# Kernel optimization log

Hardware: AMD Instinct MI355X
Metric: run time of the kernel (lower is better)

## Reference

```python
import jax, jax.numpy as jnp
import numpy as np
import math

ALPHA = math.exp(-0.001 * 1000.0)  # exp(-dt * tau_filter_inv)
T, B, D_IN, D_OUT = 2048, 32, 512, 512


def setup_inputs() -> dict:
    key = jax.random.key(0)
    k1, k2, k3 = jax.random.split(key, 3)
    bound = 1.0 / math.sqrt(D_IN)  # torch Linear default init range
    return {
        "input_tensor": jax.random.normal(k1, (T, B, D_IN), dtype=jnp.float32),
        "weight": jax.random.uniform(k2, (D_OUT, D_IN), minval=-bound, maxval=bound, dtype=jnp.float32),
        "bias": jax.random.uniform(k3, (D_OUT,), minval=-bound, maxval=bound, dtype=jnp.float32),
    }


def reference(input_tensor, weight, bias):
    # y[t] = W x[t] + b   -> [T, B, D_OUT]
    y = jnp.einsum("tbi,oi->tbo", input_tensor, weight) + bias
    alpha = jnp.asarray(ALPHA, dtype=y.dtype)

    # out[0] = y[0]; out[t] = alpha * out[t-1] + y[t]
    def step(carry, yt):
        out = alpha * carry + yt
        return out, out

    _, rest = jax.lax.scan(step, y[0], y[1:])
    return jnp.concatenate([y[:1], rest], axis=0)
```

## Files before the change

kernel.cpp:

```cpp
#include <hip/hip_runtime.h>
#include <stdint.h>

#define T_DIM 2048
#define B_DIM 32
#define DIN   512
#define DOUT  512
#define M_DIM (T_DIM * B_DIM)
#define COLS  (B_DIM * DIN)
#define COLS4 (COLS / 4)

#define ALPHA_F 0.36787944117144233f
#define INV_1MA 1.5819767068693265f

#define CHUNKS   128
#define CHUNK_T  16
#define HALO     8

#define FCHUNKS  32
#define FCHUNK_T 64
#define FHALO    16

typedef float  floatx4 __attribute__((ext_vector_type(4)));
typedef __bf16 bf16x8  __attribute__((ext_vector_type(8)));

__device__ __forceinline__ uint32_t pk2(float a, float b) {
  uint32_t ua = __float_as_uint(a); ua += 0x7fffu + ((ua >> 16) & 1u);
  uint32_t ub = __float_as_uint(b); ub += 0x7fffu + ((ub >> 16) & 1u);
  return (ua >> 16) | (ub & 0xffff0000u);
}

__device__ __forceinline__ void gload_lds16(const void* g, void* lds) {
  __builtin_amdgcn_global_load_lds(
      (const __attribute__((address_space(1))) void*)g,
      (__attribute__((address_space(3))) void*)lds,
      16, 0, 0);
}

__global__ void filter_x_kernel(const float* __restrict__ X,
                                uint16_t* __restrict__ XF,
                                const float* __restrict__ W,
                                uint16_t* __restrict__ WB)
{
  if (blockIdx.y == CHUNKS) {
    const int t = blockIdx.x * 256 + threadIdx.x;
    const float4* W4 = (const float4*)W;
#pragma unroll
    for (int j = 0; j < 8; ++j) {
      const int b4 = t * 16 + j * 2;
      float4 w0 = W4[b4], w1 = W4[b4 + 1];
      uint4 p;
      p.x = pk2(w0.x, w0.y); p.y = pk2(w0.z, w0.w);
      p.z = pk2(w1.x, w1.y); p.w = pk2(w1.z, w1.w);
      *(uint4*)&WB[t * 64 + j * 8] = p;
    }
    return;
  }

  const int col4 = blockIdx.x * blockDim.x + threadIdx.x;
  const int c = blockIdx.y;
  const float4* X4 = (const float4*)X;

  const size_t base = (size_t)c * CHUNK_T * COLS4 + col4;

  float4 h[HALO];
  float4 v[CHUNK_T];

  if (c > 0) {
    const size_t hb = base - (size_t)HALO * COLS4;
#pragma unroll
    for (int j = 0; j < HALO; ++j) h[j] = X4[hb + (size_t)j * COLS4];
  }
#pragma unroll
  for (int j = 0; j < CHUNK_T; ++j) v[j] = X4[base + (size_t)j * COLS4];

  float4 carry = {0.0f, 0.0f, 0.0f, 0.0f};
  if (c > 0) {
#pragma unroll
    for (int j = 0; j < HALO; ++j) {
      carry.x = fmaf(ALPHA_F, carry.x, h[j].x);
      carry.y = fmaf(ALPHA_F, carry.y, h[j].y);
      carry.z = fmaf(ALPHA_F, carry.z, h[j].z);
      carry.w = fmaf(ALPHA_F, carry.w, h[j].w);
    }
  }

#pragma unroll
  for (int j = 0; j < CHUNK_T; ++j) {
    carry.x = fmaf(ALPHA_F, carry.x, v[j].x);
    carry.y = fmaf(ALPHA_F, carry.y, v[j].y);
    carry.z = fmaf(ALPHA_F, carry.z, v[j].z);
    carry.w = fmaf(ALPHA_F, carry.w, v[j].w);
    uint2 p;
    p.x = pk2(carry.x, carry.y);
    p.y = pk2(carry.z, carry.w);
    *(uint2*)&XF[(base + (size_t)j * COLS4) * 4] = p;
  }
}

__launch_bounds__(256, 4)
__global__ void gemm_bf16_kernel(const uint16_t* __restrict__ XF,
                                 const uint16_t* __restrict__ WB,
                                 const float* __restrict__ bias,
                                 float* __restrict__ Y)
{
  __shared__ __align__(16) uint16_t As[128 * 64];
  __shared__ __align__(16) uint16_t Bs[128 * 64];

  const int bid = blockIdx.x;
  const int lg = (bid & 7) * 256 + (bid >> 3);
  const int n0 = (lg & 3) * 128;
  const int m0 = (lg >> 2) * 128;

  const int tid  = threadIdx.x;
  const int lane = tid & 63;
  const int w    = tid >> 6;
  const int r    = lane & 15;
  const int q    = lane >> 4;
  const int wm   = w >> 1;
  const int wn   = w & 1;

  const int srow_base = w * 32 + (lane >> 3);
  const int schunk    = lane & 7;

  floatx4 acc[4][4];
#pragma unroll
  for (int i = 0; i < 4; ++i)
#pragma unroll
    for (int j = 0; j < 4; ++j) {
      floatx4 z = {0.0f, 0.0f, 0.0f, 0.0f};
      acc[i][j] = z;
    }

  for (int kt = 0; kt < DIN / 64; ++kt) {
    const int k0 = kt * 64;
#pragma unroll
    for (int i = 0; i < 4; ++i) {
      const int row = srow_base + i * 8;
      const int sc = schunk ^ (row & 7);
      gload_lds16(XF + (size_t)(m0 + row) * DIN + k0 + sc * 8,
                  &As[(w * 32 + i * 8) * 64]);
      gload_lds16(WB + (size_t)(n0 + row) * DIN + k0 + sc * 8,
                  &Bs[(w * 32 + i * 8) * 64]);
    }
    __syncthreads();

#pragma unroll
    for (int kk = 0; kk < 2; ++kk) {
      bf16x8 af[4], bfr[4];
#pragma unroll
      for (int mi = 0; mi < 4; ++mi) {
        const int row = wm * 64 + mi * 16 + r;
        const int cch = (kk * 4 + q) ^ (row & 7);
        af[mi] = *(const bf16x8*)&As[row * 64 + (cch << 3)];
      }
#pragma unroll
      for (int ni = 0; ni < 4; ++ni) {
        const int row = wn * 64 + ni * 16 + r;
        const int cch = (kk * 4 + q) ^ (row & 7);
        bfr[ni] = *(const bf16x8*)&Bs[row * 64 + (cch << 3)];
      }
#pragma unroll
      for (int mi = 0; mi < 4; ++mi)
#pragma unroll
        for (int ni = 0; ni < 4; ++ni)
          acc[mi][ni] = __builtin_amdgcn_mfma_f32_16x16x32_bf16(
              af[mi], bfr[ni], acc[mi][ni], 0, 0, 0);
    }
    __syncthreads();
  }

#pragma unroll
  for (int mi = 0; mi < 4; ++mi) {
    const int rowb = m0 + wm * 64 + mi * 16;
    const int t = rowb >> 5;
    const float s = (1.0f - __expf(-(float)(t + 1))) * INV_1MA;
#pragma unroll
    for (int ni = 0; ni < 4; ++ni) {
      const int col = n0 + wn * 64 + ni * 16 + r;
      const float sb = s * bias[col];
#pragma unroll
      for (int j = 0; j < 4; ++j)
        Y[(size_t)(rowb + q * 4 + j) * DOUT + col] = acc[mi][ni][j] + sb;
    }
  }
}

__launch_bounds__(256, 2)
__global__ void gemm_bias_kernel(const float* __restrict__ X,
                                 const float* __restrict__ W,
                                 const float* __restrict__ bias,
                                 float* __restrict__ Y,
                                 float* __restrict__ halo,
                                 int halo_on)
{
  __shared__ __align__(16) uint16_t As[128 * 64];
  __shared__ __align__(16) uint16_t Bs[128 * 64];

  const int tid  = threadIdx.x;
  const int lane = tid & 63;
  const int wave = tid >> 6;
  const int wm   = wave >> 1;
  const int wn   = wave & 1;
  const int r    = lane & 15;
  const int q    = lane >> 4;

  const int m0 = blockIdx.y * 128;
  const int n0 = blockIdx.x * 128;

  floatx4 acc[4][4];
#pragma unroll
  for (int i = 0; i < 4; ++i)
#pragma unroll
    for (int j = 0; j < 4; ++j) {
      floatx4 z = {0.0f, 0.0f, 0.0f, 0.0f};
      acc[i][j] = z;
    }

  for (int kt = 0; kt < DIN / 64; ++kt) {
    const int k0 = kt * 64;
#pragma unroll
    for (int j = 0; j < 4; ++j) {
      const int cid = tid + j * 256;
      const int row = cid >> 3;
      const int c   = cid & 7;
      const int slot = (c ^ (row & 7)) << 3;

      const float* ga = &X[(size_t)(m0 + row) * DIN + k0 + c * 8];
      float4 a0 = *(const float4*)ga;
      float4 a1 = *(const float4*)(ga + 4);
      uint4 pa;
      pa.x = pk2(a0.x, a0.y); pa.y = pk2(a0.z, a0.w);
      pa.z = pk2(a1.x, a1.y); pa.w = pk2(a1.z, a1.w);
      *(uint4*)&As[row * 64 + slot] = pa;

      const float* gb = &W[(size_t)(n0 + row) * DIN + k0 + c * 8];
      float4 b0 = *(const float4*)gb;
      float4 b1 = *(const float4*)(gb + 4);
      uint4 pb;
      pb.x = pk2(b0.x, b0.y); pb.y = pk2(b0.z, b0.w);
      pb.z = pk2(b1.x, b1.y); pb.w = pk2(b1.z, b1.w);
      *(uint4*)&Bs[row * 64 + slot] = pb;
    }
    __syncthreads();

#pragma unroll
    for (int kk = 0; kk < 2; ++kk) {
      bf16x8 af[4], bfr[4];
#pragma unroll
      for (int mi = 0; mi < 4; ++mi) {
        const int row = wm * 64 + mi * 16 + r;
        const int c   = (kk * 4 + q) ^ (row & 7);
        af[mi] = *(const bf16x8*)&As[row * 64 + (c << 3)];
      }
#pragma unroll
      for (int ni = 0; ni < 4; ++ni) {
        const int row = wn * 64 + ni * 16 + r;
        const int c   = (kk * 4 + q) ^ (row & 7);
        bfr[ni] = *(const bf16x8*)&Bs[row * 64 + (c << 3)];
      }
#pragma unroll
      for (int mi = 0; mi < 4; ++mi)
#pragma unroll
        for (int ni = 0; ni < 4; ++ni)
          acc[mi][ni] = __builtin_amdgcn_mfma_f32_16x16x32_bf16(
              af[mi], bfr[ni], acc[mi][ni], 0, 0, 0);
    }
    __syncthreads();
  }

#pragma unroll
  for (int ni = 0; ni < 4; ++ni) {
    const int col = n0 + wn * 64 + ni * 16 + r;
    const float bv = bias[col];
#pragma unroll
    for (int mi = 0; mi < 4; ++mi) {
      const int rowm = m0 + wm * 64 + mi * 16 + q * 4;
      const int t = rowm >> 5;
      const int b = rowm & 31;
      const int tloc = t & (FCHUNK_T - 1);
      const bool hw = halo_on && (tloc >= FCHUNK_T - FHALO) && (t < T_DIM - FCHUNK_T);
      const size_t hbase = hw
          ? ((size_t)(((t >> 6) + 1) * FHALO + (tloc - (FCHUNK_T - FHALO))) * COLS)
          : 0;
#pragma unroll
      for (int j = 0; j < 4; ++j) {
        const float v = acc[mi][ni][j] + bv;
        Y[(size_t)(rowm + j) * DOUT + col] = v;
        if (hw) halo[hbase + (size_t)(b + j) * DOUT + col] = v;
      }
    }
  }
}

__global__ void scan_kernel(float* __restrict__ Y,
                            const float* __restrict__ halo,
                            int chunk_len)
{
  const int col4 = blockIdx.x * blockDim.x + threadIdx.x;
  const int c = blockIdx.y;

  float4* Y4 = (float4*)Y;
  const float4* H4 = (const float4*)halo;

  float4 carry = {0.0f, 0.0f, 0.0f, 0.0f};
  if (c > 0) {
#pragma unroll
    for (int h = 0; h < FHALO; ++h) {
      float4 v = H4[(size_t)(c * FHALO + h) * COLS4 + col4];
      carry.x = fmaf(ALPHA_F, carry.x, v.x);
      carry.y = fmaf(ALPHA_F, carry.y, v.y);
      carry.z = fmaf(ALPHA_F, carry.z, v.z);
      carry.w = fmaf(ALPHA_F, carry.w, v.w);
    }
  }

  size_t idx = (size_t)c * chunk_len * COLS4 + col4;
  float4 ynext = Y4[idx];
  for (int t = 0; t < chunk_len; ++t) {
    float4 y = ynext;
    if (t + 1 < chunk_len) ynext = Y4[idx + COLS4];
    carry.x = fmaf(ALPHA_F, carry.x, y.x);
    carry.y = fmaf(ALPHA_F, carry.y, y.y);
    carry.z = fmaf(ALPHA_F, carry.z, y.z);
    carry.w = fmaf(ALPHA_F, carry.w, y.w);
    Y4[idx] = carry;
    idx += COLS4;
  }
}

extern "C" void kernel_launch(void* const* d_in, const int* in_sizes, int n_in,
                              void* d_out, int out_size, void* d_ws, size_t ws_size,
                              hipStream_t stream)
{
  const float* X    = (const float*)d_in[0];
  const float* W    = (const float*)d_in[1];
  const float* bias = (const float*)d_in[2];
  float* Y = (float*)d_out;

  const size_t need_new = (size_t)M_DIM * DIN * 2 + (size_t)DOUT * DIN * 2;

  if (ws_size >= need_new) {
    uint16_t* XF = (uint16_t*)d_ws;
    uint16_t* WB = XF + (size_t)M_DIM * DIN;

    dim3 gf(16, CHUNKS + 1);
    filter_x_kernel<<<gf, 256, 0, stream>>>(X, XF, W, WB);

    gemm_bf16_kernel<<<2048, 256, 0, stream>>>(XF, WB, bias, Y);
  } else {
    float* halo = (float*)d_ws;
    const size_t halo_need = (size_t)FCHUNKS * FHALO * COLS * sizeof(float);
    const int halo_on = (ws_size >= halo_need) ? 1 : 0;

    dim3 g1(DOUT / 128, M_DIM / 128);
    gemm_bias_kernel<<<g1, 256, 0, stream>>>(X, W, bias, Y, halo, halo_on);

    const int n_chunks = halo_on ? FCHUNKS : 1;
    dim3 g2(COLS4 / 256, n_chunks);
    scan_kernel<<<g2, 256, 0, stream>>>(Y, halo, T_DIM / n_chunks);
  }
}
```

Baseline: 98.09 us.

## Fuse input prefilter into GEMM A-tile load, dropping the XF intermediate

```diff
diff --git a/kernel.cpp b/kernel.cpp
--- a/kernel.cpp
+++ b/kernel.cpp
@@ -12,9 +12,7 @@
 #define ALPHA_F 0.36787944117144233f
 #define INV_1MA 1.5819767068693265f
 
-#define CHUNKS   128
-#define CHUNK_T  16
-#define HALO     8
+#define HALO 8
 
 #define FCHUNKS  32
 #define FCHUNK_T 64
@@ -36,72 +34,27 @@
       16, 0, 0);
 }
 
-__global__ void filter_x_kernel(const float* __restrict__ X,
-                                uint16_t* __restrict__ XF,
-                                const float* __restrict__ W,
-                                uint16_t* __restrict__ WB)
-{
-  if (blockIdx.y == CHUNKS) {
-    const int t = blockIdx.x * 256 + threadIdx.x;
-    const float4* W4 = (const float4*)W;
-#pragma unroll
-    for (int j = 0; j < 8; ++j) {
-      const int b4 = t * 16 + j * 2;
-      float4 w0 = W4[b4], w1 = W4[b4 + 1];
-      uint4 p;
-      p.x = pk2(w0.x, w0.y); p.y = pk2(w0.z, w0.w);
-      p.z = pk2(w1.x, w1.y); p.w = pk2(w1.z, w1.w);
-      *(uint4*)&WB[t * 64 + j * 8] = p;
-    }
-    return;
-  }
-
-  const int col4 = blockIdx.x * blockDim.x + threadIdx.x;
-  const int c = blockIdx.y;
-  const float4* X4 = (const float4*)X;
-
-  const size_t base = (size_t)c * CHUNK_T * COLS4 + col4;
-
-  float4 h[HALO];
-  float4 v[CHUNK_T];
-
-  if (c > 0) {
-    const size_t hb = base - (size_t)HALO * COLS4;
-#pragma unroll
-    for (int j = 0; j < HALO; ++j) h[j] = X4[hb + (size_t)j * COLS4];
-  }
-#pragma unroll
-  for (int j = 0; j < CHUNK_T; ++j) v[j] = X4[base + (size_t)j * COLS4];
-
-  float4 carry = {0.0f, 0.0f, 0.0f, 0.0f};
-  if (c > 0) {
-#pragma unroll
-    for (int j = 0; j < HALO; ++j) {
-      carry.x = fmaf(ALPHA_F, carry.x, h[j].x);
-      carry.y = fmaf(ALPHA_F, carry.y, h[j].y);
-      carry.z = fmaf(ALPHA_F, carry.z, h[j].z);
-      carry.w = fmaf(ALPHA_F, carry.w, h[j].w);
-    }
-  }
-
-#pragma unroll
-  for (int j = 0; j < CHUNK_T; ++j) {
-    carry.x = fmaf(ALPHA_F, carry.x, v[j].x);
-    carry.y = fmaf(ALPHA_F, carry.y, v[j].y);
-    carry.z = fmaf(ALPHA_F, carry.z, v[j].z);
-    carry.w = fmaf(ALPHA_F, carry.w, v[j].w);
-    uint2 p;
-    p.x = pk2(carry.x, carry.y);
-    p.y = pk2(carry.z, carry.w);
-    *(uint2*)&XF[(base + (size_t)j * COLS4) * 4] = p;
-  }
-}
-
-__launch_bounds__(256, 4)
-__global__ void gemm_bf16_kernel(const uint16_t* __restrict__ XF,
-                                 const uint16_t* __restrict__ WB,
-                                 const float* __restrict__ bias,
-                                 float* __restrict__ Y)
+__global__ void wconv_kernel(const float* __restrict__ W,
+                             uint16_t* __restrict__ WB)
+{
+  const int t = blockIdx.x * 256 + threadIdx.x;
+  const float4* W4 = (const float4*)W;
+#pragma unroll
+  for (int j = 0; j < 8; ++j) {
+    const int b4 = t * 16 + j * 2;
+    float4 w0 = W4[b4], w1 = W4[b4 + 1];
+    uint4 p;
+    p.x = pk2(w0.x, w0.y); p.y = pk2(w0.z, w0.w);
+    p.z = pk2(w1.x, w1.y); p.w = pk2(w1.z, w1.w);
+    *(uint4*)&WB[t * 64 + j * 8] = p;
+  }
+}
+
+__launch_bounds__(256, 2)
+__global__ void fused_filter_gemm_kernel(const float* __restrict__ X,
+                                         const uint16_t* __restrict__ WB,
+                                         const float* __restrict__ bias,
+                                         float* __restrict__ Y)
 {
   __shared__ __align__(16) uint16_t As[128 * 64];
   __shared__ __align__(16) uint16_t Bs[128 * 64];
@@ -110,6 +63,7 @@
   const int lg = (bid & 7) * 256 + (bid >> 3);
   const int n0 = (lg & 3) * 128;
   const int m0 = (lg >> 2) * 128;
+  const int t0 = m0 >> 5;
 
   const int tid  = threadIdx.x;
   const int lane = tid & 63;
@@ -119,9 +73,15 @@
   const int wm   = w >> 1;
   const int wn   = w & 1;
 
+  const int b_   = tid >> 3;
+  const int oct  = tid & 7;
+  const int aslot = (oct ^ (b_ & 7)) << 3;
+
   const int srow_base = w * 32 + (lane >> 3);
   const int schunk    = lane & 7;
 
+  const float4* X4 = (const float4*)X;
+
   floatx4 acc[4][4];
 #pragma unroll
   for (int i = 0; i < 4; ++i)
@@ -131,17 +91,59 @@
       acc[i][j] = z;
     }
 
+  const float4 zero4 = {0.0f, 0.0f, 0.0f, 0.0f};
+
   for (int kt = 0; kt < DIN / 64; ++kt) {
-    const int k0 = kt * 64;
+    const int k4 = kt * 16;
+
 #pragma unroll
     for (int i = 0; i < 4; ++i) {
       const int row = srow_base + i * 8;
       const int sc = schunk ^ (row & 7);
-      gload_lds16(XF + (size_t)(m0 + row) * DIN + k0 + sc * 8,
-                  &As[(w * 32 + i * 8) * 64]);
-      gload_lds16(WB + (size_t)(n0 + row) * DIN + k0 + sc * 8,
+      gload_lds16(WB + (size_t)(n0 + row) * DIN + kt * 64 + sc * 8,
                   &Bs[(w * 32 + i * 8) * 64]);
     }
+
+    float4 hx0[HALO], hx1[HALO];
+#pragma unroll
+    for (int j = 0; j < HALO; ++j) {
+      const int t = t0 - HALO + j;
+      if (t >= 0) {
+        const size_t f4 = (size_t)(t * 32 + b_) * 128 + k4 + oct * 2;
+        hx0[j] = X4[f4];
+        hx1[j] = X4[f4 + 1];
+      } else {
+        hx0[j] = zero4; hx1[j] = zero4;
+      }
+    }
+    float4 mx0[4], mx1[4];
+#pragma unroll
+    for (int j = 0; j < 4; ++j) {
+      const size_t f4 = (size_t)((t0 + j) * 32 + b_) * 128 + k4 + oct * 2;
+      mx0[j] = X4[f4];
+      mx1[j] = X4[f4 + 1];
+    }
+
+    float4 c0 = zero4, c1 = zero4;
+#pragma unroll
+    for (int j = 0; j < HALO; ++j) {
+      c0.x = fmaf(ALPHA_F, c0.x, hx0[j].x); c0.y = fmaf(ALPHA_F, c0.y, hx0[j].y);
+      c0.z = fmaf(ALPHA_F, c0.z, hx0[j].z); c0.w = fmaf(ALPHA_F, c0.w, hx0[j].w);
+      c1.x = fmaf(ALPHA_F, c1.x, hx1[j].x); c1.y = fmaf(ALPHA_F, c1.y, hx1[j].y);
+      c1.z = fmaf(ALPHA_F, c1.z, hx1[j].z); c1.w = fmaf(ALPHA_F, c1.w, hx1[j].w);
+    }
+#pragma unroll
+    for (int j = 0; j < 4; ++j) {
+      c0.x = fmaf(ALPHA_F, c0.x, mx0[j].x); c0.y = fmaf(ALPHA_F, c0.y, mx0[j].y);
+      c0.z = fmaf(ALPHA_F, c0.z, mx0[j].z); c0.w = fmaf(ALPHA_F, c0.w, mx0[j].w);
+      c1.x = fmaf(ALPHA_F, c1.x, mx1[j].x); c1.y = fmaf(ALPHA_F, c1.y, mx1[j].y);
+      c1.z = fmaf(ALPHA_F, c1.z, mx1[j].z); c1.w = fmaf(ALPHA_F, c1.w, mx1[j].w);
+      uint4 p;
+      p.x = pk2(c0.x, c0.y); p.y = pk2(c0.z, c0.w);
+      p.z = pk2(c1.x, c1.y); p.w = pk2(c1.z, c1.w);
+      *(uint4*)&As[(j * 32 + b_) * 64 + aslot] = p;
+    }
+
     __syncthreads();
 
 #pragma unroll
@@ -337,16 +339,12 @@
   const float* bias = (const float*)d_in[2];
   float* Y = (float*)d_out;
 
-  const size_t need_new = (size_t)M_DIM * DIN * 2 + (size_t)DOUT * DIN * 2;
-
-  if (ws_size >= need_new) {
-    uint16_t* XF = (uint16_t*)d_ws;
-    uint16_t* WB = XF + (size_t)M_DIM * DIN;
-
-    dim3 gf(16, CHUNKS + 1);
-    filter_x_kernel<<<gf, 256, 0, stream>>>(X, XF, W, WB);
-
-    gemm_bf16_kernel<<<2048, 256, 0, stream>>>(XF, WB, bias, Y);
+  const size_t need_wb = (size_t)DOUT * DIN * 2;
+
+  if (ws_size >= need_wb) {
+    uint16_t* WB = (uint16_t*)d_ws;
+    wconv_kernel<<<16, 256, 0, stream>>>(W, WB);
+    fused_filter_gemm_kernel<<<2048, 256, 0, stream>>>(X, WB, bias, Y);
   } else {
     float* halo = (float*)d_ws;
     const size_t halo_need = (size_t)FCHUNKS * FHALO * COLS * sizeof(float);
```

Result: slower. 142.9 us (+45.7%).

## Stream filter loads through a ring buffer, halve chunk count, split weight conversion

Applied to the files above, without the earlier changes.

```diff
diff --git a/kernel.cpp b/kernel.cpp
--- a/kernel.cpp
+++ b/kernel.cpp
@@ -12,8 +12,8 @@
 #define ALPHA_F 0.36787944117144233f
 #define INV_1MA 1.5819767068693265f
 
-#define CHUNKS   128
-#define CHUNK_T  16
+#define CHUNKS   64
+#define CHUNK_T  32
 #define HALO     8
 
 #define FCHUNKS  32
@@ -36,65 +36,68 @@
       16, 0, 0);
 }
 
+__device__ __forceinline__ void fma4(float4& c, const float4& v) {
+  c.x = fmaf(ALPHA_F, c.x, v.x);
+  c.y = fmaf(ALPHA_F, c.y, v.y);
+  c.z = fmaf(ALPHA_F, c.z, v.z);
+  c.w = fmaf(ALPHA_F, c.w, v.w);
+}
+
+__global__ void wconv_kernel(const float* __restrict__ W,
+                             uint16_t* __restrict__ WB)
+{
+  const int t = blockIdx.x * 256 + threadIdx.x;
+  const float4* W4 = (const float4*)W;
+#pragma unroll
+  for (int j = 0; j < 8; ++j) {
+    const int b4 = t * 16 + j * 2;
+    float4 w0 = W4[b4], w1 = W4[b4 + 1];
+    uint4 p;
+    p.x = pk2(w0.x, w0.y); p.y = pk2(w0.z, w0.w);
+    p.z = pk2(w1.x, w1.y); p.w = pk2(w1.z, w1.w);
+    *(uint4*)&WB[t * 64 + j * 8] = p;
+  }
+}
+
+template<bool HAS_HALO>
+__device__ __forceinline__ void filter_chunk(const float4* __restrict__ X4,
+                                             uint16_t* __restrict__ XF,
+                                             size_t base)
+{
+  constexpr int NSTEP = HAS_HALO ? (CHUNK_T + HALO) : CHUNK_T;
+  const size_t b0 = HAS_HALO ? (base - (size_t)HALO * COLS4) : base;
+
+  float4 ring[4];
+  float4 carry = {0.0f, 0.0f, 0.0f, 0.0f};
+
+#pragma unroll
+  for (int j = 0; j < 4; ++j) ring[j] = X4[b0 + (size_t)j * COLS4];
+
+#pragma unroll
+  for (int s = 0; s < NSTEP; ++s) {
+    float4 v = ring[s & 3];
+    if (s + 4 < NSTEP) ring[s & 3] = X4[b0 + (size_t)(s + 4) * COLS4];
+    fma4(carry, v);
+    const int t = HAS_HALO ? (s - HALO) : s;
+    if (t >= 0) {
+      uint2 p;
+      p.x = pk2(carry.x, carry.y);
+      p.y = pk2(carry.z, carry.w);
+      *(uint2*)&XF[(base + (size_t)t * COLS4) * 4] = p;
+    }
+  }
+}
+
 __global__ void filter_x_kernel(const float* __restrict__ X,
-                                uint16_t* __restrict__ XF,
-                                const float* __restrict__ W,
-                                uint16_t* __restrict__ WB)
-{
-  if (blockIdx.y == CHUNKS) {
-    const int t = blockIdx.x * 256 + threadIdx.x;
-    const float4* W4 = (const float4*)W;
-#pragma unroll
-    for (int j = 0; j < 8; ++j) {
-      const int b4 = t * 16 + j * 2;
-      float4 w0 = W4[b4], w1 = W4[b4 + 1];
-      uint4 p;
-      p.x = pk2(w0.x, w0.y); p.y = pk2(w0.z, w0.w);
-      p.z = pk2(w1.x, w1.y); p.w = pk2(w1.z, w1.w);
-      *(uint4*)&WB[t * 64 + j * 8] = p;
-    }
-    return;
-  }
-
-  const int col4 = blockIdx.x * blockDim.x + threadIdx.x;
+                                uint16_t* __restrict__ XF)
+{
+  const int col4 = blockIdx.x * 256 + threadIdx.x;
   const int c = blockIdx.y;
   const float4* X4 = (const float4*)X;
-
   const size_t base = (size_t)c * CHUNK_T * COLS4 + col4;
 
-  float4 h[HALO];
-  float4 v[CHUNK_T];
-
-  if (c > 0) {
-    const size_t hb = base - (size_t)HALO * COLS4;
-#pragma unroll
-    for (int j = 0; j < HALO; ++j) h[j] = X4[hb + (size_t)j * COLS4];
-  }
-#pragma unroll
-  for (int j = 0; j < CHUNK_T; ++j) v[j] = X4[base + (size_t)j * COLS4];
-
-  float4 carry = {0.0f, 0.0f, 0.0f, 0.0f};
-  if (c > 0) {
-#pragma unroll
-    for (int j = 0; j < HALO; ++j) {
-      carry.x = fmaf(ALPHA_F, carry.x, h[j].x);
-      carry.y = fmaf(ALPHA_F, carry.y, h[j].y);
-      carry.z = fmaf(ALPHA_F, carry.z, h[j].z);
-      carry.w = fmaf(ALPHA_F, carry.w, h[j].w);
-    }
-  }
-
-#pragma unroll
-  for (int j = 0; j < CHUNK_T; ++j) {
-    carry.x = fmaf(ALPHA_F, carry.x, v[j].x);
-    carry.y = fmaf(ALPHA_F, carry.y, v[j].y);
-    carry.z = fmaf(ALPHA_F, carry.z, v[j].z);
-    carry.w = fmaf(ALPHA_F, carry.w, v[j].w);
-    uint2 p;
-    p.x = pk2(carry.x, carry.y);
-    p.y = pk2(carry.z, carry.w);
-    *(uint2*)&XF[(base + (size_t)j * COLS4) * 4] = p;
-  }
+  if (c > 0) filter_chunk<true>(X4, XF, base);
+  else       filter_chunk<false>(X4, XF, base);
 }
 
 __launch_bounds__(256, 4)
@@ -194,7 +197,7 @@
                                  int halo_on)
 {
   __shared__ __align__(16) uint16_t As[128 * 64];
-  __shared__ __align__(16) uint16_t Bs[128 * 64];
+  __shared__ __align__(16) uint16_t Bsh[128 * 64];
 
   const int tid  = threadIdx.x;
   const int lane = tid & 63;
@@ -239,7 +242,7 @@
       uint4 pb;
       pb.x = pk2(b0.x, b0.y); pb.y = pk2(b0.z, b0.w);
       pb.z = pk2(b1.x, b1.y); pb.w = pk2(b1.z, b1.w);
-      *(uint4*)&Bs[row * 64 + slot] = pb;
+      *(uint4*)&Bsh[row * 64 + slot] = pb;
     }
     __syncthreads();
 
@@ -256,7 +259,7 @@
       for (int ni = 0; ni < 4; ++ni) {
         const int row = wn * 64 + ni * 16 + r;
         const int c   = (kk * 4 + q) ^ (row & 7);
-        bfr[ni] = *(const bf16x8*)&Bs[row * 64 + (c << 3)];
+        bfr[ni] = *(const bf16x8*)&Bsh[row * 64 + (c << 3)];
       }
 #pragma unroll
       for (int mi = 0; mi < 4; ++mi)
@@ -307,10 +310,7 @@
 #pragma unroll
     for (int h = 0; h < FHALO; ++h) {
       float4 v = H4[(size_t)(c * FHALO + h) * COLS4 + col4];
-      carry.x = fmaf(ALPHA_F, carry.x, v.x);
-      carry.y = fmaf(ALPHA_F, carry.y, v.y);
-      carry.z = fmaf(ALPHA_F, carry.z, v.z);
-      carry.w = fmaf(ALPHA_F, carry.w, v.w);
+      fma4(carry, v);
     }
   }
 
@@ -319,10 +319,7 @@
   for (int t = 0; t < chunk_len; ++t) {
     float4 y = ynext;
     if (t + 1 < chunk_len) ynext = Y4[idx + COLS4];
-    carry.x = fmaf(ALPHA_F, carry.x, y.x);
-    carry.y = fmaf(ALPHA_F, carry.y, y.y);
-    carry.z = fmaf(ALPHA_F, carry.z, y.z);
-    carry.w = fmaf(ALPHA_F, carry.w, y.w);
+    fma4(carry, y);
     Y4[idx] = carry;
     idx += COLS4;
   }
@@ -343,9 +340,9 @@
     uint16_t* XF = (uint16_t*)d_ws;
     uint16_t* WB = XF + (size_t)M_DIM * DIN;
 
-    dim3 gf(16, CHUNKS + 1);
-    filter_x_kernel<<<gf, 256, 0, stream>>>(X, XF, W, WB);
-
+    wconv_kernel<<<16, 256, 0, stream>>>(W, WB);
+    dim3 gf(16, CHUNKS);
+    filter_x_kernel<<<gf, 256, 0, stream>>>(X, XF);
     gemm_bf16_kernel<<<2048, 256, 0, stream>>>(XF, WB, bias, Y);
   } else {
     float* halo = (float*)d_ws;
```

Result: slower. 106.2 us (+8.3%).
